# Kernel tuning notes

Measured on AMD Instinct MI355X. Metric: run time of the kernel, lower is better.

The kernel has to match this reference:

```python
import jax, jax.numpy as jnp
import numpy as np

BEAM_WIDTH = 4
BLANK_INDEX = 0
EOS_INDEX = 1


def setup_inputs():
    key = jax.random.key(0)
    k1, k2 = jax.random.split(key)
    T, B, C = 128, 8, 25000
    logits = jax.random.normal(k1, (T, B, C), dtype=jnp.float32)
    seq_len = jnp.full((B,), T, dtype=jnp.int32)
    return {"logits": logits, "seq_len": seq_len}


def _beam_search(logits):
    # logits: [T, B, C]; vectorized form of the per-step beam update:
    #   softmax(beam_score + logits) over C, top-k over (beam, char),
    #   backpointer gather of sequences, per-step re-sort by cumulative log score.
    T, B, C = logits.shape
    W = BEAM_WIDTH
    seqs0 = jnp.full((B, W, T + 1), BLANK_INDEX, dtype=jnp.int32)
    scores0 = jnp.zeros((B, W), dtype=logits.dtype)  # per-step softmax prob score
    logs0 = jnp.zeros((B, W), dtype=logits.dtype)    # accumulated log prob
    active0 = jnp.zeros((B, W), dtype=bool).at[:, 0].set(True)  # start with one beam

    def step(carry, xs):
        scores, logs, seqs, active = carry
        logit_t, t = xs
        # beam score is ADDED to logits before softmax (matches original math)
        expanded = scores[:, :, None] + logit_t[:, None, :]          # [B, W, C]
        probs = jax.nn.softmax(expanded, axis=-1)
        probs = jnp.where(active[:, :, None], probs, -1.0)           # mask inactive beams
        top_p, top_i = jax.lax.top_k(probs.reshape(B, W * C), W)      # [B, W]
        beam_idx = top_i // C                                        # backpointers
        char = (top_i % C).astype(jnp.int32)
        new_logs = jnp.take_along_axis(logs, beam_idx, axis=1) + jnp.log(top_p)
        new_seqs = jnp.take_along_axis(seqs, beam_idx[:, :, None], axis=1)
        # eos is dropped from the sequence in the original; represent as blank
        char_w = jnp.where(char == EOS_INDEX, BLANK_INDEX, char)
        new_seqs = new_seqs.at[:, :, t + 1].set(char_w)
        # per-step re-sort of surviving beams by cumulative log score (desc)
        order = jnp.argsort(-new_logs, axis=1)
        top_p = jnp.take_along_axis(top_p, order, axis=1)
        new_logs = jnp.take_along_axis(new_logs, order, axis=1)
        new_seqs = jnp.take_along_axis(new_seqs, order[:, :, None], axis=1)
        return (top_p, new_logs, new_seqs, jnp.ones_like(active)), None

    (scores, logs, seqs, _), _ = jax.lax.scan(
        step, (scores0, logs0, seqs0, active0), (logits, jnp.arange(T)))
    # final sort by last-step prob score (original sorts by x[0] at the end)
    order = jnp.argsort(-scores, axis=1)
    scores = jnp.take_along_axis(scores, order, axis=1)
    logs = jnp.take_along_axis(logs, order, axis=1)
    seqs = jnp.take_along_axis(seqs, order[:, :, None], axis=1)
    return seqs, scores, logs


def reference(logits, seq_len):
    seqs, scores, logs = _beam_search(logits)
    return seqs, scores, logs
```

## Files before the change

### kernel.cpp

```cpp
#include <hip/hip_runtime.h>
#include <math.h>

#define T_ 128
#define B_ 8
#define C_ 25000
#define W_ 4
#define NROWS (T_ * B_)
#define NT4 (C_ / 4)

__device__ __forceinline__ bool better(float av, int ai, float bv, int bi) {
  return (av > bv) || (av == bv && ai < bi);
}

__global__ __launch_bounds__(512) void rowstats(
    const float* __restrict__ logits,
    double* __restrict__ d_lp0, double* __restrict__ d_p0,
    int* __restrict__ d_ci0, int* __restrict__ d_tied,
    float* __restrict__ d_t4v, int* __restrict__ d_t4i,
    double* __restrict__ d_t4lp, double* __restrict__ d_t4p) {
  const int row = blockIdx.x;
  const float4* __restrict__ x4 =
      reinterpret_cast<const float4*>(logits + (size_t)row * C_);
  const int tid = threadIdx.x;

  float m1 = -INFINITY, m2 = -INFINITY;
  int idx = 0;
  float s0 = 0.0f, s1 = 0.0f;

#pragma unroll 4
  for (int i = tid; i < NT4; i += 512) {
    float4 q = x4[i];
    const int gi = 4 * i;
    s0 += __expf(q.x) + __expf(q.y);
    s1 += __expf(q.z) + __expf(q.w);
    { bool c = q.x > m1; m2 = fmaxf(m2, fminf(q.x, m1));
      idx = c ? (gi + 0) : idx; m1 = fmaxf(m1, q.x); }
    { bool c = q.y > m1; m2 = fmaxf(m2, fminf(q.y, m1));
      idx = c ? (gi + 1) : idx; m1 = fmaxf(m1, q.y); }
    { bool c = q.z > m1; m2 = fmaxf(m2, fminf(q.z, m1));
      idx = c ? (gi + 2) : idx; m1 = fmaxf(m1, q.z); }
    { bool c = q.w > m1; m2 = fmaxf(m2, fminf(q.w, m1));
      idx = c ? (gi + 3) : idx; m1 = fmaxf(m1, q.w); }
  }

  double sumd = (double)s0 + (double)s1;
#pragma unroll
  for (int d = 1; d < 64; d <<= 1) {
    float om1 = __shfl_xor(m1, d, 64);
    float om2 = __shfl_xor(m2, d, 64);
    int oidx = __shfl_xor(idx, d, 64);
    double osum = __shfl_xor(sumd, d, 64);
    sumd += osum;
    float nm2 = fmaxf(fminf(m1, om1), fmaxf(m2, om2));
    bool take = (om1 > m1) || (om1 == m1 && oidx < idx);
    m1 = take ? om1 : m1;
    idx = take ? oidx : idx;
    m2 = nm2;
  }

  __shared__ float g_m1[8], g_m2[8];
  __shared__ int g_idx[8];
  __shared__ double g_sum[8];
  __shared__ double sh_logden;
  __shared__ int sh_phase2;
  if ((tid & 63) == 0) {
    int w = tid >> 6;
    g_m1[w] = m1; g_m2[w] = m2; g_idx[w] = idx; g_sum[w] = sumd;
  }
  __syncthreads();

  if (tid == 0) {
    float M1 = g_m1[0], M2 = g_m2[0];
    int I = g_idx[0];
    double S = g_sum[0];
#pragma unroll
    for (int w = 1; w < 8; ++w) {
      S += g_sum[w];
      float b1 = g_m1[w], b2 = g_m2[w];
      float nm2 = fmaxf(fminf(M1, b1), fmaxf(M2, b2));
      bool take = (b1 > M1) || (b1 == M1 && g_idx[w] < I);
      if (take) { M1 = b1; I = g_idx[w]; }
      M2 = nm2;
    }
    const int t = row / B_, b = row % B_;
    const int orow = b * T_ + t;
    double logden = log(S);
    double lp0 = (double)M1 - logden;
    d_lp0[orow] = lp0;
    d_p0[orow] = exp(lp0);
    d_ci0[orow] = I;
    int tied = (__float_as_uint(M1) == __float_as_uint(M2)) ? 1 : 0;
    d_tied[orow] = tied;
    sh_logden = logden;
    sh_phase2 = tied | (t == 0 ? 1 : 0);
  }
  __syncthreads();

  if (!sh_phase2) return;

  float tv[4] = {-INFINITY, -INFINITY, -INFINITY, -INFINITY};
  int ti4[4] = {0x7fffffff, 0x7fffffff, 0x7fffffff, 0x7fffffff};
  auto ins = [&](float cv, int ci2) {
#pragma unroll
    for (int k = 0; k < 4; ++k) {
      if (better(cv, ci2, tv[k], ti4[k])) {
        float t0 = tv[k]; int t1 = ti4[k];
        tv[k] = cv; ti4[k] = ci2;
        cv = t0; ci2 = t1;
      }
    }
  };
  for (int i = tid; i < NT4; i += 512) {
    float4 q = x4[i];
    const int gi = 4 * i;
    if (better(q.x, gi + 0, tv[3], ti4[3])) ins(q.x, gi + 0);
    if (better(q.y, gi + 1, tv[3], ti4[3])) ins(q.y, gi + 1);
    if (better(q.z, gi + 2, tv[3], ti4[3])) ins(q.z, gi + 2);
    if (better(q.w, gi + 3, tv[3], ti4[3])) ins(q.w, gi + 3);
  }

  __shared__ float sv[512][4];
  __shared__ int si[512][4];
#pragma unroll
  for (int k = 0; k < 4; ++k) { sv[tid][k] = tv[k]; si[tid][k] = ti4[k]; }
  __syncthreads();

  for (int off = 256; off > 0; off >>= 1) {
    if (tid < off) {
      float a0[4], ov[4]; int a1[4], oi[4];
#pragma unroll
      for (int k = 0; k < 4; ++k) { a0[k] = sv[tid][k]; a1[k] = si[tid][k]; }
      int pa = 0, pb = 0;
#pragma unroll
      for (int k = 0; k < 4; ++k) {
        float bv_ = sv[tid + off][pb]; int bi_ = si[tid + off][pb];
        if (better(a0[pa], a1[pa], bv_, bi_)) { ov[k] = a0[pa]; oi[k] = a1[pa]; ++pa; }
        else { ov[k] = bv_; oi[k] = bi_; ++pb; }
      }
#pragma unroll
      for (int k = 0; k < 4; ++k) { sv[tid][k] = ov[k]; si[tid][k] = oi[k]; }
    }
    __syncthreads();
  }

  if (tid == 0) {
    const int t = row / B_, b = row % B_;
    const int orow = b * T_ + t;
    double logden = sh_logden;
#pragma unroll
    for (int k = 0; k < 4; ++k) {
      d_t4v[orow * 4 + k] = sv[0][k];
      d_t4i[orow * 4 + k] = si[0][k];
      double lp = (double)sv[0][k] - logden;
      d_t4lp[orow * 4 + k] = lp;
      d_t4p[orow * 4 + k] = exp(lp);
    }
  }
}

__global__ __launch_bounds__(64) void beam_sim(
    const double* __restrict__ d_lp0, const double* __restrict__ d_p0,
    const int* __restrict__ d_ci0, const int* __restrict__ d_tied,
    const float* __restrict__ d_t4v, const int* __restrict__ d_t4i,
    const double* __restrict__ d_t4lp, const double* __restrict__ d_t4p,
    float* __restrict__ out) {
  const int b = blockIdx.x;
  const int tid = threadIdx.x;

  __shared__ double lp0[T_], p0v[T_];
  __shared__ int ci0[T_], tiedL[T_];
  __shared__ double S[T_];
  __shared__ int Pst[T_][4], Chst[T_][4];
  __shared__ int seq[W_][T_];
  __shared__ double sh_scores[W_], sh_logs[W_];
  __shared__ int sh_ford[W_];

  const int base = b * T_;
  for (int e = tid; e < T_; e += 64) {
    lp0[e] = d_lp0[base + e];
    p0v[e] = d_p0[base + e];
    ci0[e] = d_ci0[base + e];
    tiedL[e] = d_tied[base + e];
  }
  __syncthreads();

  bool slA = (tid >= 1) && (tiedL[tid] != 0);
  bool slB = (tiedL[tid + 64] != 0);
  const unsigned long long mask0 = __ballot(slA);
  const unsigned long long mask1 = __ballot(slB);

  {
    const int t0 = 2 * tid, t1 = 2 * tid + 1;
    double e0 = (t0 >= 1) ? lp0[t0] : 0.0;
    double e1 = lp0[t1];
    double pair = e0 + e1;
    double sc = pair;
#pragma unroll
    for (int d = 1; d < 64; d <<= 1) {
      double o = __shfl_up(sc, d, 64);
      if (tid >= d) sc += o;
    }
    double excl = sc - pair;
    S[t0] = excl + e0;
    S[t1] = sc;
  }

  for (int t = tid + 1; t < T_; t += 64) {
    bool slow = (t < 64) ? ((mask0 >> t) & 1ull) : ((mask1 >> (t - 64)) & 1ull);
    if (!slow) {
      int c = ci0[t];
      seq[0][t] = c; seq[1][t] = c; seq[2][t] = c; seq[3][t] = c;
    }
  }
  __syncthreads();

  if (tid == 0) {
    double logs[4], scor[4] = {0.0, 0.0, 0.0, 0.0};
    const int base4 = base * 4;
    for (int j = 0; j < 4; ++j) logs[j] = d_t4lp[base4 + j];
    int tprev = 0, lastSlow = -1;

    unsigned long long mm = mask0;
    int phase = 0;
    while (true) {
      if (mm == 0) {
        if (phase == 0) { mm = mask1; phase = 1; continue; }
        break;
      }
      int bpos = __builtin_ctzll(mm); mm &= mm - 1;
      int ts = bpos + (phase ? 64 : 0);

      double add = S[ts - 1] - S[tprev];
      for (int j = 0; j < 4; ++j) logs[j] += add;

      const int row4 = (base + ts) * 4;
      float v[4]; int ci[4]; double lpk4[4], pk4[4];
      for (int k = 0; k < 4; ++k) {
        v[k] = d_t4v[row4 + k];
        ci[k] = d_t4i[row4 + k];
        lpk4[k] = d_t4lp[row4 + k];
        pk4[k] = d_t4p[row4 + k];
      }
      int sw[4], sc_[4], sk[4]; int ns = 0; int k = 0;
      while (ns < 4 && k < 4) {
        int k2 = k;
        while (k2 + 1 < 4 &&
               __float_as_uint(v[k2 + 1]) == __float_as_uint(v[k])) ++k2;
        for (int w = 0; w < 4 && ns < 4; ++w)
          for (int kk = k; kk <= k2 && ns < 4; ++kk) {
            sw[ns] = w; sc_[ns] = ci[kk]; sk[ns] = kk; ++ns;
          }
        k = k2 + 1;
      }
      double nl[4];
      for (int j = 0; j < 4; ++j) nl[j] = logs[sw[j]] + lpk4[sk[j]];
      int ord[4] = {0, 1, 2, 3};
      for (int a = 1; a < 4; ++a) {
        int o = ord[a]; int bb = a;
        while (bb > 0 && nl[ord[bb - 1]] < nl[o]) { ord[bb] = ord[bb - 1]; --bb; }
        ord[bb] = o;
      }
      for (int j = 0; j < 4; ++j) {
        Pst[ts][j] = sw[ord[j]];
        Chst[ts][j] = sc_[ord[j]];
      }
      double tl[4];
      for (int j = 0; j < 4; ++j) tl[j] = nl[ord[j]];
      for (int j = 0; j < 4; ++j) logs[j] = tl[j];
      if (ts == T_ - 1)
        for (int j = 0; j < 4; ++j) scor[j] = pk4[sk[ord[j]]];
      tprev = ts;
      lastSlow = ts;
    }
    double add = S[T_ - 1] - S[tprev];
    for (int j = 0; j < 4; ++j) logs[j] += add;
    if (lastSlow != T_ - 1)
      for (int j = 0; j < 4; ++j) scor[j] = p0v[T_ - 1];

    float sf[4];
    for (int j = 0; j < 4; ++j) sf[j] = (float)scor[j];
    int ford[4] = {0, 1, 2, 3};
    for (int a = 1; a < 4; ++a) {
      int o = ford[a]; int bb = a;
      while (bb > 0 && sf[ford[bb - 1]] < sf[o]) { ford[bb] = ford[bb - 1]; --bb; }
      ford[bb] = o;
    }
    for (int w = 0; w < 4; ++w) {
      sh_ford[w] = ford[w];
      sh_scores[w] = scor[ford[w]];
      sh_logs[w] = logs[ford[w]];
    }
  }
  __syncthreads();

  if (tid < W_) {
    int j = sh_ford[tid];
    unsigned long long mm = mask1;
    int phase = 1;
    while (true) {
      if (mm == 0) {
        if (phase == 1) { mm = mask0; phase = 0; continue; }
        break;
      }
      int bpos = 63 - __builtin_clzll(mm); mm &= ~(1ull << bpos);
      int ts = bpos + (phase ? 64 : 0);
      seq[tid][ts] = Chst[ts][j];
      j = Pst[ts][j];
    }
    seq[tid][0] = d_t4i[base * 4 + j];
  }
  __syncthreads();

  for (int e = tid; e < W_ * (T_ + 1); e += 64) {
    int w = e / (T_ + 1), p = e % (T_ + 1);
    int c = (p == 0) ? 0 : seq[w][p - 1];
    if (c == 1) c = 0;
    out[(size_t)(b * W_ + w) * (T_ + 1) + p] = (float)c;
  }
  if (tid < W_) {
    out[B_ * W_ * (T_ + 1) + b * W_ + tid] = (float)sh_scores[tid];
    out[B_ * W_ * (T_ + 1) + B_ * W_ + b * W_ + tid] = (float)sh_logs[tid];
  }
}

extern "C" void kernel_launch(void* const* d_in, const int* in_sizes, int n_in,
                              void* d_out, int out_size, void* d_ws,
                              size_t ws_size, hipStream_t stream) {
  const float* logits = (const float*)d_in[0];

  char* ws = (char*)d_ws;
  double* d_lp0 = (double*)(ws + 0);
  double* d_p0 = (double*)(ws + 8192);
  double* d_t4lp = (double*)(ws + 16384);
  double* d_t4p = (double*)(ws + 49152);
  int* d_ci0 = (int*)(ws + 81920);
  int* d_tied = (int*)(ws + 86016);
  float* d_t4v = (float*)(ws + 90112);
  int* d_t4i = (int*)(ws + 106496);
  float* out = (float*)d_out;

  hipLaunchKernelGGL(rowstats, dim3(NROWS), dim3(512), 0, stream,
                     logits, d_lp0, d_p0, d_ci0, d_tied,
                     d_t4v, d_t4i, d_t4lp, d_t4p);
  hipLaunchKernelGGL(beam_sim, dim3(B_), dim3(64), 0, stream,
                     d_lp0, d_p0, d_ci0, d_tied,
                     d_t4v, d_t4i, d_t4lp, d_t4p, out);
}
```

Measured before the change: 41.72 us.

## Fuse row statistics and beam simulation into one kernel via last-block counter

```diff
diff --git a/kernel.cpp b/kernel.cpp
--- a/kernel.cpp
+++ b/kernel.cpp
@@ -7,43 +7,75 @@
 #define W_ 4
 #define NROWS (T_ * B_)
 #define NT4 (C_ / 4)
+#define TAILQ (NT4 - 512 * 12)
+#define SEQ_ELEMS (B_ * W_ * (T_ + 1))
+
+#define WS_DEN   0
+#define WS_M1    8192
+#define WS_I0    12288
+#define WS_TIED  16384
+#define WS_T4V   20480
+#define WS_T4I   36864
+#define WS_PCH   53248
+#define WS_CNT   69632
 
 __device__ __forceinline__ bool better(float av, int ai, float bv, int bi) {
   return (av > bv) || (av == bv && ai < bi);
 }
 
-__global__ __launch_bounds__(512) void rowstats(
-    const float* __restrict__ logits,
-    double* __restrict__ d_lp0, double* __restrict__ d_p0,
-    int* __restrict__ d_ci0, int* __restrict__ d_tied,
-    float* __restrict__ d_t4v, int* __restrict__ d_t4i,
-    double* __restrict__ d_t4lp, double* __restrict__ d_t4p) {
+__global__ __launch_bounds__(512, 8) void fused_kernel(
+    const float* __restrict__ logits, char* __restrict__ ws,
+    float* __restrict__ out) {
+  double* d_den = (double*)(ws + WS_DEN);
+  float* d_m1 = (float*)(ws + WS_M1);
+  int* d_i0 = (int*)(ws + WS_I0);
+  int* d_tied = (int*)(ws + WS_TIED);
+  float* d_t4v = (float*)(ws + WS_T4V);
+  int* d_t4i = (int*)(ws + WS_T4I);
+  unsigned* pch_g = (unsigned*)(ws + WS_PCH);
+  int* counter = (int*)(ws + WS_CNT);
+
+  __shared__ char smem[29312] __attribute__((aligned(16)));
+  __shared__ float g_m1[8], g_m2[8];
+  __shared__ int g_idx[8];
+  __shared__ double g_sum[8];
+  __shared__ int sh_phase2, sh_last;
+
   const int row = blockIdx.x;
-  const float4* __restrict__ x4 =
-      reinterpret_cast<const float4*>(logits + (size_t)row * C_);
   const int tid = threadIdx.x;
+  const float4* __restrict__ x4 = (const float4*)(logits + (size_t)row * C_);
 
   float m1 = -INFINITY, m2 = -INFINITY;
-  int idx = 0;
-  float s0 = 0.0f, s1 = 0.0f;
-
-#pragma unroll 4
-  for (int i = tid; i < NT4; i += 512) {
-    float4 q = x4[i];
-    const int gi = 4 * i;
-    s0 += __expf(q.x) + __expf(q.y);
-    s1 += __expf(q.z) + __expf(q.w);
-    { bool c = q.x > m1; m2 = fmaxf(m2, fminf(q.x, m1));
-      idx = c ? (gi + 0) : idx; m1 = fmaxf(m1, q.x); }
-    { bool c = q.y > m1; m2 = fmaxf(m2, fminf(q.y, m1));
-      idx = c ? (gi + 1) : idx; m1 = fmaxf(m1, q.y); }
-    { bool c = q.z > m1; m2 = fmaxf(m2, fminf(q.z, m1));
-      idx = c ? (gi + 2) : idx; m1 = fmaxf(m1, q.z); }
-    { bool c = q.w > m1; m2 = fmaxf(m2, fminf(q.w, m1));
-      idx = c ? (gi + 3) : idx; m1 = fmaxf(m1, q.w); }
-  }
-
-  double sumd = (double)s0 + (double)s1;
+  int iq = 0, ij = 0;
+  float s0 = 0.f, s1 = 0.f, s2 = 0.f, s3 = 0.f;
+
+  auto consume = [&](const float4 q, int i) {
+    { bool c = q.x > m1; m2 = __builtin_amdgcn_fmed3f(q.x, m1, m2);
+      m1 = fmaxf(m1, q.x); iq = c ? i : iq; ij = c ? 0 : ij; s0 += __expf(q.x); }
+    { bool c = q.y > m1; m2 = __builtin_amdgcn_fmed3f(q.y, m1, m2);
+      m1 = fmaxf(m1, q.y); iq = c ? i : iq; ij = c ? 1 : ij; s1 += __expf(q.y); }
+    { bool c = q.z > m1; m2 = __builtin_amdgcn_fmed3f(q.z, m1, m2);
+      m1 = fmaxf(m1, q.z); iq = c ? i : iq; ij = c ? 2 : ij; s2 += __expf(q.z); }
+    { bool c = q.w > m1; m2 = __builtin_amdgcn_fmed3f(q.w, m1, m2);
+      m1 = fmaxf(m1, q.w); iq = c ? i : iq; ij = c ? 3 : ij; s3 += __expf(q.w); }
+  };
+
+#pragma unroll
+  for (int kb = 0; kb < 3; ++kb) {
+    float4 q[4];
+    const int i0 = tid + 512 * 4 * kb;
+#pragma unroll
+    for (int k = 0; k < 4; ++k) q[k] = x4[i0 + 512 * k];
+#pragma unroll
+    for (int k = 0; k < 4; ++k) consume(q[k], i0 + 512 * k);
+  }
+  if (tid < TAILQ) {
+    float4 q = x4[tid + 512 * 12];
+    consume(q, tid + 512 * 12);
+  }
+  int idx = iq * 4 + ij;
+
+  double sumd = (double)(s0 + s1) + (double)(s2 + s3);
 #pragma unroll
   for (int d = 1; d < 64; d <<= 1) {
     float om1 = __shfl_xor(m1, d, 64);
@@ -57,22 +89,16 @@
     idx = take ? oidx : idx;
     m2 = nm2;
   }
-
-  __shared__ float g_m1[8], g_m2[8];
-  __shared__ int g_idx[8];
-  __shared__ double g_sum[8];
-  __shared__ double sh_logden;
-  __shared__ int sh_phase2;
   if ((tid & 63) == 0) {
     int w = tid >> 6;
     g_m1[w] = m1; g_m2[w] = m2; g_idx[w] = idx; g_sum[w] = sumd;
   }
   __syncthreads();
 
+  const int t = row / B_, b = row % B_;
+  const int orow = b * T_ + t;
   if (tid == 0) {
-    float M1 = g_m1[0], M2 = g_m2[0];
-    int I = g_idx[0];
-    double S = g_sum[0];
+    float M1 = g_m1[0], M2 = g_m2[0]; int I = g_idx[0]; double S = g_sum[0];
 #pragma unroll
     for (int w = 1; w < 8; ++w) {
       S += g_sum[w];
@@ -82,173 +108,162 @@
       if (take) { M1 = b1; I = g_idx[w]; }
       M2 = nm2;
     }
-    const int t = row / B_, b = row % B_;
-    const int orow = b * T_ + t;
-    double logden = log(S);
-    double lp0 = (double)M1 - logden;
-    d_lp0[orow] = lp0;
-    d_p0[orow] = exp(lp0);
-    d_ci0[orow] = I;
+    d_den[orow] = S;
+    d_m1[orow] = M1;
+    d_i0[orow] = I;
     int tied = (__float_as_uint(M1) == __float_as_uint(M2)) ? 1 : 0;
     d_tied[orow] = tied;
-    sh_logden = logden;
     sh_phase2 = tied | (t == 0 ? 1 : 0);
   }
   __syncthreads();
 
-  if (!sh_phase2) return;
-
-  float tv[4] = {-INFINITY, -INFINITY, -INFINITY, -INFINITY};
-  int ti4[4] = {0x7fffffff, 0x7fffffff, 0x7fffffff, 0x7fffffff};
-  auto ins = [&](float cv, int ci2) {
-#pragma unroll
-    for (int k = 0; k < 4; ++k) {
-      if (better(cv, ci2, tv[k], ti4[k])) {
-        float t0 = tv[k]; int t1 = ti4[k];
-        tv[k] = cv; ti4[k] = ci2;
-        cv = t0; ci2 = t1;
-      }
-    }
-  };
-  for (int i = tid; i < NT4; i += 512) {
-    float4 q = x4[i];
-    const int gi = 4 * i;
-    if (better(q.x, gi + 0, tv[3], ti4[3])) ins(q.x, gi + 0);
-    if (better(q.y, gi + 1, tv[3], ti4[3])) ins(q.y, gi + 1);
-    if (better(q.z, gi + 2, tv[3], ti4[3])) ins(q.z, gi + 2);
-    if (better(q.w, gi + 3, tv[3], ti4[3])) ins(q.w, gi + 3);
-  }
-
-  __shared__ float sv[512][4];
-  __shared__ int si[512][4];
-#pragma unroll
-  for (int k = 0; k < 4; ++k) { sv[tid][k] = tv[k]; si[tid][k] = ti4[k]; }
-  __syncthreads();
-
-  for (int off = 256; off > 0; off >>= 1) {
-    if (tid < off) {
-      float a0[4], ov[4]; int a1[4], oi[4];
-#pragma unroll
-      for (int k = 0; k < 4; ++k) { a0[k] = sv[tid][k]; a1[k] = si[tid][k]; }
-      int pa = 0, pb = 0;
+  if (sh_phase2) {
+    float* sv = (float*)smem;
+    int* si = (int*)(smem + 8192);
+    float tv[4] = {-INFINITY, -INFINITY, -INFINITY, -INFINITY};
+    int ti4[4] = {0x7fffffff, 0x7fffffff, 0x7fffffff, 0x7fffffff};
+    auto ins = [&](float cv, int ci2) {
 #pragma unroll
       for (int k = 0; k < 4; ++k) {
-        float bv_ = sv[tid + off][pb]; int bi_ = si[tid + off][pb];
-        if (better(a0[pa], a1[pa], bv_, bi_)) { ov[k] = a0[pa]; oi[k] = a1[pa]; ++pa; }
-        else { ov[k] = bv_; oi[k] = bi_; ++pb; }
-      }
-#pragma unroll
-      for (int k = 0; k < 4; ++k) { sv[tid][k] = ov[k]; si[tid][k] = oi[k]; }
-    }
+        if (better(cv, ci2, tv[k], ti4[k])) {
+          float t0 = tv[k]; int t1 = ti4[k];
+          tv[k] = cv; ti4[k] = ci2;
+          cv = t0; ci2 = t1;
+        }
+      }
+    };
+    for (int i = tid; i < NT4; i += 512) {
+      float4 q = x4[i];
+      const int gi = 4 * i;
+      if (better(q.x, gi + 0, tv[3], ti4[3])) ins(q.x, gi + 0);
+      if (better(q.y, gi + 1, tv[3], ti4[3])) ins(q.y, gi + 1);
+      if (better(q.z, gi + 2, tv[3], ti4[3])) ins(q.z, gi + 2);
+      if (better(q.w, gi + 3, tv[3], ti4[3])) ins(q.w, gi + 3);
+    }
+#pragma unroll
+    for (int k = 0; k < 4; ++k) { sv[tid * 4 + k] = tv[k]; si[tid * 4 + k] = ti4[k]; }
     __syncthreads();
+    for (int off = 256; off > 0; off >>= 1) {
+      if (tid < off) {
+        float a0[4], ov[4]; int a1[4], oi[4];
+#pragma unroll
+        for (int k = 0; k < 4; ++k) { a0[k] = sv[tid * 4 + k]; a1[k] = si[tid * 4 + k]; }
+        int pa = 0, pb = 0;
+#pragma unroll
+        for (int k = 0; k < 4; ++k) {
+          float bv_ = sv[(tid + off) * 4 + pb]; int bi_ = si[(tid + off) * 4 + pb];
+          if (better(a0[pa], a1[pa], bv_, bi_)) { ov[k] = a0[pa]; oi[k] = a1[pa]; ++pa; }
+          else { ov[k] = bv_; oi[k] = bi_; ++pb; }
+        }
+#pragma unroll
+        for (int k = 0; k < 4; ++k) { sv[tid * 4 + k] = ov[k]; si[tid * 4 + k] = oi[k]; }
+      }
+      __syncthreads();
+    }
+    if (tid == 0) {
+#pragma unroll
+      for (int k = 0; k < 4; ++k) {
+        d_t4v[orow * 4 + k] = sv[k];
+        d_t4i[orow * 4 + k] = si[k];
+      }
+    }
+    __syncthreads();
   }
 
   if (tid == 0) {
-    const int t = row / B_, b = row % B_;
-    const int orow = b * T_ + t;
-    double logden = sh_logden;
-#pragma unroll
-    for (int k = 0; k < 4; ++k) {
-      d_t4v[orow * 4 + k] = sv[0][k];
-      d_t4i[orow * 4 + k] = si[0][k];
-      double lp = (double)sv[0][k] - logden;
-      d_t4lp[orow * 4 + k] = lp;
-      d_t4p[orow * 4 + k] = exp(lp);
-    }
-  }
-}
-
-__global__ __launch_bounds__(64) void beam_sim(
-    const double* __restrict__ d_lp0, const double* __restrict__ d_p0,
-    const int* __restrict__ d_ci0, const int* __restrict__ d_tied,
-    const float* __restrict__ d_t4v, const int* __restrict__ d_t4i,
-    const double* __restrict__ d_t4lp, const double* __restrict__ d_t4p,
-    float* __restrict__ out) {
-  const int b = blockIdx.x;
-  const int tid = threadIdx.x;
-
-  __shared__ double lp0[T_], p0v[T_];
-  __shared__ int ci0[T_], tiedL[T_];
-  __shared__ double S[T_];
-  __shared__ int Pst[T_][4], Chst[T_][4];
-  __shared__ int seq[W_][T_];
-  __shared__ double sh_scores[W_], sh_logs[W_];
-  __shared__ int sh_ford[W_];
-
-  const int base = b * T_;
-  for (int e = tid; e < T_; e += 64) {
-    lp0[e] = d_lp0[base + e];
-    p0v[e] = d_p0[base + e];
-    ci0[e] = d_ci0[base + e];
-    tiedL[e] = d_tied[base + e];
-  }
-  __syncthreads();
-
-  bool slA = (tid >= 1) && (tiedL[tid] != 0);
-  bool slB = (tiedL[tid + 64] != 0);
+    __threadfence();
+    int old = atomicAdd(counter, 1);
+    sh_last = (old == NROWS - 1) ? 1 : 0;
+  }
+  __syncthreads();
+  if (!sh_last) return;
+  __threadfence();
+  __syncthreads();
+
+  double* lp0a = (double*)smem;
+  double* Sa = (double*)(smem + 8192);
+  int* ci0a = (int*)(smem + 16384);
+  unsigned short* seqa = (unsigned short*)(smem + 20480);
+  double* scoresa = (double*)(smem + 28672);
+  double* logsa = (double*)(smem + 28928);
+  int* forda = (int*)(smem + 29184);
+
+  for (int r = tid; r < NROWS; r += 512) {
+    lp0a[r] = (double)d_m1[r] - log(d_den[r]);
+    ci0a[r] = d_i0[r];
+  }
+  __syncthreads();
+
+  const int wv = tid >> 6;
+  const int lane = tid & 63;
+  const int bb = wv;
+  const int basep = bb * T_;
+
+  bool slA = (lane >= 1) && (d_tied[basep + lane] != 0);
+  bool slB = (d_tied[basep + 64 + lane] != 0);
   const unsigned long long mask0 = __ballot(slA);
   const unsigned long long mask1 = __ballot(slB);
 
   {
-    const int t0 = 2 * tid, t1 = 2 * tid + 1;
-    double e0 = (t0 >= 1) ? lp0[t0] : 0.0;
-    double e1 = lp0[t1];
-    double pair = e0 + e1;
-    double sc = pair;
+    const int t0 = 2 * lane, t1 = 2 * lane + 1;
+    double e0 = (t0 >= 1) ? lp0a[basep + t0] : 0.0;
+    double e1 = lp0a[basep + t1];
+    double pair = e0 + e1, sc = pair;
 #pragma unroll
     for (int d = 1; d < 64; d <<= 1) {
       double o = __shfl_up(sc, d, 64);
-      if (tid >= d) sc += o;
-    }
-    double excl = sc - pair;
-    S[t0] = excl + e0;
-    S[t1] = sc;
-  }
-
-  for (int t = tid + 1; t < T_; t += 64) {
-    bool slow = (t < 64) ? ((mask0 >> t) & 1ull) : ((mask1 >> (t - 64)) & 1ull);
+      if (lane >= d) sc += o;
+    }
+    Sa[basep + t0] = sc - pair + e0;
+    Sa[basep + t1] = sc;
+  }
+
+  for (int t2 = lane + 1; t2 < T_; t2 += 64) {
+    bool slow = (t2 < 64) ? ((mask0 >> t2) & 1ull) : ((mask1 >> (t2 - 64)) & 1ull);
     if (!slow) {
-      int c = ci0[t];
-      seq[0][t] = c; seq[1][t] = c; seq[2][t] = c; seq[3][t] = c;
-    }
-  }
-  __syncthreads();
-
-  if (tid == 0) {
+      unsigned short c = (unsigned short)ci0a[basep + t2];
+      seqa[(bb * 4 + 0) * T_ + t2] = c;
+      seqa[(bb * 4 + 1) * T_ + t2] = c;
+      seqa[(bb * 4 + 2) * T_ + t2] = c;
+      seqa[(bb * 4 + 3) * T_ + t2] = c;
+    }
+  }
+  __syncthreads();
+
+  if (lane == 0) {
     double logs[4], scor[4] = {0.0, 0.0, 0.0, 0.0};
-    const int base4 = base * 4;
-    for (int j = 0; j < 4; ++j) logs[j] = d_t4lp[base4 + j];
+    {
+      double lden0 = log(d_den[basep]);
+      for (int j = 0; j < 4; ++j)
+        logs[j] = (double)d_t4v[basep * 4 + j] - lden0;
+    }
     int tprev = 0, lastSlow = -1;
-
-    unsigned long long mm = mask0;
-    int phase = 0;
+    unsigned long long mm = mask0; int phase = 0;
     while (true) {
-      if (mm == 0) {
-        if (phase == 0) { mm = mask1; phase = 1; continue; }
-        break;
-      }
+      if (mm == 0) { if (phase == 0) { mm = mask1; phase = 1; continue; } break; }
       int bpos = __builtin_ctzll(mm); mm &= mm - 1;
       int ts = bpos + (phase ? 64 : 0);
 
-      double add = S[ts - 1] - S[tprev];
+      double add = Sa[basep + ts - 1] - Sa[basep + tprev];
       for (int j = 0; j < 4; ++j) logs[j] += add;
 
-      const int row4 = (base + ts) * 4;
+      const int row4 = (basep + ts) * 4;
       float v[4]; int ci[4]; double lpk4[4], pk4[4];
+      double lden = log(d_den[basep + ts]);
       for (int k = 0; k < 4; ++k) {
         v[k] = d_t4v[row4 + k];
         ci[k] = d_t4i[row4 + k];
-        lpk4[k] = d_t4lp[row4 + k];
-        pk4[k] = d_t4p[row4 + k];
+        lpk4[k] = (double)v[k] - lden;
+        pk4[k] = exp(lpk4[k]);
       }
       int sw[4], sc_[4], sk[4]; int ns = 0; int k = 0;
       while (ns < 4 && k < 4) {
         int k2 = k;
         while (k2 + 1 < 4 &&
                __float_as_uint(v[k2 + 1]) == __float_as_uint(v[k])) ++k2;
-        for (int w = 0; w < 4 && ns < 4; ++w)
+        for (int w2 = 0; w2 < 4 && ns < 4; ++w2)
           for (int kk = k; kk <= k2 && ns < 4; ++kk) {
-            sw[ns] = w; sc_[ns] = ci[kk]; sk[ns] = kk; ++ns;
+            sw[ns] = w2; sc_[ns] = ci[kk]; sk[ns] = kk; ++ns;
           }
         k = k2 + 1;
       }
@@ -256,14 +271,13 @@
       for (int j = 0; j < 4; ++j) nl[j] = logs[sw[j]] + lpk4[sk[j]];
       int ord[4] = {0, 1, 2, 3};
       for (int a = 1; a < 4; ++a) {
-        int o = ord[a]; int bb = a;
-        while (bb > 0 && nl[ord[bb - 1]] < nl[o]) { ord[bb] = ord[bb - 1]; --bb; }
-        ord[bb] = o;
-      }
-      for (int j = 0; j < 4; ++j) {
-        Pst[ts][j] = sw[ord[j]];
-        Chst[ts][j] = sc_[ord[j]];
-      }
+        int o = ord[a]; int bq = a;
+        while (bq > 0 && nl[ord[bq - 1]] < nl[o]) { ord[bq] = ord[bq - 1]; --bq; }
+        ord[bq] = o;
+      }
+      for (int j = 0; j < 4; ++j)
+        pch_g[(basep + ts) * 4 + j] =
+            ((unsigned)sw[ord[j]] << 16) | (unsigned)sc_[ord[j]];
       double tl[4];
       for (int j = 0; j < 4; ++j) tl[j] = nl[ord[j]];
       for (int j = 0; j < 4; ++j) logs[j] = tl[j];
@@ -272,54 +286,53 @@
       tprev = ts;
       lastSlow = ts;
     }
-    double add = S[T_ - 1] - S[tprev];
+    double add = Sa[basep + T_ - 1] - Sa[basep + tprev];
     for (int j = 0; j < 4; ++j) logs[j] += add;
-    if (lastSlow != T_ - 1)
-      for (int j = 0; j < 4; ++j) scor[j] = p0v[T_ - 1];
+    if (lastSlow != T_ - 1) {
+      double pl = exp(lp0a[basep + T_ - 1]);
+      for (int j = 0; j < 4; ++j) scor[j] = pl;
+    }
 
     float sf[4];
     for (int j = 0; j < 4; ++j) sf[j] = (float)scor[j];
     int ford[4] = {0, 1, 2, 3};
     for (int a = 1; a < 4; ++a) {
-      int o = ford[a]; int bb = a;
-      while (bb > 0 && sf[ford[bb - 1]] < sf[o]) { ford[bb] = ford[bb - 1]; --bb; }
-      ford[bb] = o;
-    }
-    for (int w = 0; w < 4; ++w) {
-      sh_ford[w] = ford[w];
-      sh_scores[w] = scor[ford[w]];
-      sh_logs[w] = logs[ford[w]];
-    }
-  }
-  __syncthreads();
-
-  if (tid < W_) {
-    int j = sh_ford[tid];
-    unsigned long long mm = mask1;
-    int phase = 1;
+      int o = ford[a]; int bq = a;
+      while (bq > 0 && sf[ford[bq - 1]] < sf[o]) { ford[bq] = ford[bq - 1]; --bq; }
+      ford[bq] = o;
+    }
+    for (int w2 = 0; w2 < 4; ++w2) {
+      forda[bb * 4 + w2] = ford[w2];
+      scoresa[bb * 4 + w2] = scor[ford[w2]];
+      logsa[bb * 4 + w2] = logs[ford[w2]];
+    }
+  }
+  __syncthreads();
+
+  if (lane < W_) {
+    int j = forda[bb * 4 + lane];
+    unsigned long long mm = mask1; int phase = 1;
     while (true) {
-      if (mm == 0) {
-        if (phase == 1) { mm = mask0; phase = 0; continue; }
-        break;
-      }
+      if (mm == 0) { if (phase == 1) { mm = mask0; phase = 0; continue; } break; }
       int bpos = 63 - __builtin_clzll(mm); mm &= ~(1ull << bpos);
       int ts = bpos + (phase ? 64 : 0);
-      seq[tid][ts] = Chst[ts][j];
-      j = Pst[ts][j];
-    }
-    seq[tid][0] = d_t4i[base * 4 + j];
-  }
-  __syncthreads();
-
-  for (int e = tid; e < W_ * (T_ + 1); e += 64) {
-    int w = e / (T_ + 1), p = e % (T_ + 1);
-    int c = (p == 0) ? 0 : seq[w][p - 1];
+      unsigned pc = pch_g[(basep + ts) * 4 + j];
+      seqa[(bb * 4 + lane) * T_ + ts] = (unsigned short)(pc & 0xFFFFu);
+      j = (int)(pc >> 16);
+    }
+    seqa[(bb * 4 + lane) * T_ + 0] = (unsigned short)d_t4i[basep * 4 + j];
+  }
+  __syncthreads();
+
+  for (int e = lane; e < W_ * (T_ + 1); e += 64) {
+    int w2 = e / (T_ + 1), p = e % (T_ + 1);
+    int c = (p == 0) ? 0 : (int)seqa[(bb * 4 + w2) * T_ + (p - 1)];
     if (c == 1) c = 0;
-    out[(size_t)(b * W_ + w) * (T_ + 1) + p] = (float)c;
-  }
-  if (tid < W_) {
-    out[B_ * W_ * (T_ + 1) + b * W_ + tid] = (float)sh_scores[tid];
-    out[B_ * W_ * (T_ + 1) + B_ * W_ + b * W_ + tid] = (float)sh_logs[tid];
+    out[(size_t)(bb * W_ + w2) * (T_ + 1) + p] = (float)c;
+  }
+  if (lane < W_) {
+    out[SEQ_ELEMS + bb * W_ + lane] = (float)scoresa[bb * 4 + lane];
+    out[SEQ_ELEMS + B_ * W_ + bb * W_ + lane] = (float)logsa[bb * 4 + lane];
   }
 }
 
@@ -327,22 +340,11 @@
                               void* d_out, int out_size, void* d_ws,
                               size_t ws_size, hipStream_t stream) {
   const float* logits = (const float*)d_in[0];
-
   char* ws = (char*)d_ws;
-  double* d_lp0 = (double*)(ws + 0);
-  double* d_p0 = (double*)(ws + 8192);
-  double* d_t4lp = (double*)(ws + 16384);
-  double* d_t4p = (double*)(ws + 49152);
-  int* d_ci0 = (int*)(ws + 81920);
-  int* d_tied = (int*)(ws + 86016);
-  float* d_t4v = (float*)(ws + 90112);
-  int* d_t4i = (int*)(ws + 106496);
   float* out = (float*)d_out;
 
-  hipLaunchKernelGGL(rowstats, dim3(NROWS), dim3(512), 0, stream,
-                     logits, d_lp0, d_p0, d_ci0, d_tied,
-                     d_t4v, d_t4i, d_t4lp, d_t4p);
-  hipLaunchKernelGGL(beam_sim, dim3(B_), dim3(64), 0, stream,
-                     d_lp0, d_p0, d_ci0, d_tied,
-                     d_t4v, d_t4i, d_t4lp, d_t4p, out);
+  hipMemsetAsync(ws + WS_CNT, 0, sizeof(int), stream);
+
+  hipLaunchKernelGGL(fused_kernel, dim3(NROWS), dim3(512), 0, stream,
+                     logits, ws, out);
 }
```

Result: slower. 85.53 us (+105.0%).
